# Performance work log

Measured on AMD Instinct MI355X. Metric: run time of the kernel, lower is better.

## Reference

```python
import jax, jax.numpy as jnp
import numpy as np

N, D, NUM_CLASSES = 8192, 1024, 128
ALPHA = 0.1
EPS = 1e-7


def setup_inputs() -> dict:
    key = jax.random.key(0)
    k1, k2 = jax.random.split(key)
    H = jax.random.normal(k1, (N, D), dtype=jnp.float32)
    labels = jax.random.randint(k2, (N,), 0, NUM_CLASSES, dtype=jnp.int64)
    return {"H": H, "labels": labels}


def reference(H, labels):
    n = H.shape[0]
    # squared-euclidean pairwise distances: ||x_i - x_j||^2
    x_norm = jnp.sum(H * H, axis=1)                      # [N]
    dists = x_norm[:, None] + x_norm[None, :] - 2.0 * (H @ H.T)
    dists = jnp.where(jnp.isnan(dists), 0.0, dists)      # dist[dist != dist] = 0
    dists = jnp.maximum(dists, 0.0)                      # clamp(0, inf)
    dists = jnp.maximum(dists, EPS)                      # clamp(min=1e-7)

    diffs = labels[None, :] - labels[:, None]            # [N, N]
    eye = jnp.eye(n, dtype=bool)
    mask_pos = (diffs == 0) & ~eye                       # same label, not self
    mask_neg = diffs != 0                                # different label

    # hardest positive: argmax over positive-masked distances
    anchor_positive_dist = jnp.where(mask_pos, dists, 0.0)
    hardest_positive_idx = jnp.argmax(anchor_positive_dist, axis=1)

    # hard negative: add row-max to non-negatives, take 2nd-smallest (k=1 partition)
    max_neg = jnp.max(dists, axis=1, keepdims=True)
    anchor_negative_dist = dists + max_neg * (1.0 - mask_neg.astype(dists.dtype))
    _, idx2 = jax.lax.top_k(-anchor_negative_dist, 2)    # two smallest per row
    hardest_negatives_idx = idx2[:, 1]

    rows = jnp.arange(n)
    hardest_positive_dist = dists[rows, hardest_positive_idx]
    hardest_negative_dist = dists[rows, hardest_negatives_idx]
    differences = hardest_positive_dist - hardest_negative_dist

    triplet_loss = jnp.maximum(differences + ALPHA, 0.0)  # final='plus', do_max=True
    relevant = triplet_loss > EPS                          # boolean mask (no grad)
    count = jnp.sum(relevant.astype(triplet_loss.dtype))
    return jnp.sum(jnp.where(relevant, triplet_loss, 0.0)) / count
```

## Files before the change

### kernel.cpp

```cpp
#include <hip/hip_runtime.h>
#include <hip/hip_bf16.h>
#include <stdint.h>

constexpr int Nn = 8192;
constexpr int Dd = 1024;
constexpr float kAlpha = 0.1f;
constexpr float kEps = 1e-7f;
constexpr float kInf = 3.0e38f;

constexpr int BM = 128, BN = 128, BK = 32;
constexpr int NB = Nn / BM;
constexpr int NPAIR = NB * (NB + 1) / 2;

using bfx8 = __attribute__((ext_vector_type(8))) __bf16;
using f32x4 = __attribute__((ext_vector_type(4))) float;

__device__ __forceinline__ unsigned short f2bf(float f) {
  union { float f; unsigned int u; } v; v.f = f;
  unsigned int u = v.u;
  u = u + 0x7fffu + ((u >> 16) & 1u);
  return (unsigned short)(u >> 16);
}

__device__ __forceinline__ void min2_insert(float& m1, float& m2, float x) {
  const float lo = fminf(m1, x);
  const float hi = fmaxf(m1, x);
  m1 = lo;
  m2 = fminf(m2, hi);
}

__device__ __forceinline__ void min2_merge(float& m1, float& m2, float o1, float o2) {
  m2 = fminf(fminf(m2, o2), fmaxf(m1, o1));
  m1 = fminf(m1, o1);
}

__global__ __launch_bounds__(256) void prep_kernel(const float* __restrict__ H,
                                                   unsigned short* __restrict__ Hb,
                                                   float* __restrict__ xn) {
  const int wave = threadIdx.x >> 6;
  const int lane = threadIdx.x & 63;
  const int row = blockIdx.x * 4 + wave;
  const float4* src = (const float4*)(H + (size_t)row * Dd);
  ushort4* dst = (ushort4*)(Hb + (size_t)row * Dd);
  float acc = 0.f;
#pragma unroll
  for (int i = 0; i < 4; ++i) {
    float4 v = src[lane + 64 * i];
    acc = fmaf(v.x, v.x, acc);
    acc = fmaf(v.y, v.y, acc);
    acc = fmaf(v.z, v.z, acc);
    acc = fmaf(v.w, v.w, acc);
    ushort4 o;
    o.x = f2bf(v.x); o.y = f2bf(v.y); o.z = f2bf(v.z); o.w = f2bf(v.w);
    dst[lane + 64 * i] = o;
  }
#pragma unroll
  for (int off = 32; off; off >>= 1) acc += __shfl_xor(acc, off, 64);
  if (lane == 0) xn[row] = acc;
}

__global__ __launch_bounds__(256, 3) void triplet_main(
    const unsigned short* __restrict__ Hb, const float* __restrict__ xn,
    const int* __restrict__ lab, float* __restrict__ wsMax,
    float* __restrict__ wsM1, float* __restrict__ wsM2) {
  __shared__ __align__(16) unsigned char smem[16384];
  unsigned short* As = (unsigned short*)smem;
  unsigned short* Bs = (unsigned short*)(smem + 8192);

  const int tid = threadIdx.x;
  const int wave = tid >> 6;
  const int lane = tid & 63;
  const int quad = lane >> 4;
  const int l15 = lane & 15;
  const int wm = wave & 1;
  const int wn = wave >> 1;

  int b = blockIdx.x, I = 0;
  while (b >= NB - I) { b -= NB - I; ++I; }
  const int J = I + b;
  const bool diag = (I == J);

  const int rowBase = I * BM;
  const int colBase = J * BN;

  int lr[16]; float xr[16];
#pragma unroll
  for (int m = 0; m < 4; ++m)
#pragma unroll
    for (int r = 0; r < 4; ++r) {
      const int row = rowBase + wm * 64 + m * 16 + quad * 4 + r;
      lr[m * 4 + r] = lab[row];
      xr[m * 4 + r] = xn[row];
    }

  float maxp[16], mn1[16], mn2[16];
#pragma unroll
  for (int s = 0; s < 16; ++s) { maxp[s] = 0.f; mn1[s] = kInf; mn2[s] = kInf; }

  const int stRow = wave * 32 + (lane >> 2);
  const int stCol = (lane & 3) * 8;

  f32x4 acc[4][4];
#pragma unroll
  for (int m = 0; m < 4; ++m)
#pragma unroll
    for (int n = 0; n < 4; ++n) acc[m][n] = {0.f, 0.f, 0.f, 0.f};

  for (int kt = 0; kt < Dd; kt += BK) {
    __syncthreads();
#pragma unroll
    for (int j = 0; j < 2; ++j) {
      const unsigned short* ga =
          Hb + (size_t)(rowBase + stRow + j * 16) * Dd + kt + stCol;
      __builtin_amdgcn_global_load_lds(
          (const __attribute__((address_space(1))) void*)ga,
          (__attribute__((address_space(3))) void*)&As[(wave * 2 + j) * 512],
          16, 0, 0);
      const unsigned short* gb =
          Hb + (size_t)(colBase + stRow + j * 16) * Dd + kt + stCol;
      __builtin_amdgcn_global_load_lds(
          (const __attribute__((address_space(1))) void*)gb,
          (__attribute__((address_space(3))) void*)&Bs[(wave * 2 + j) * 512],
          16, 0, 0);
    }
    __syncthreads();

    bfx8 a[4], bb[4];
#pragma unroll
    for (int m = 0; m < 4; ++m)
      a[m] = *(const bfx8*)&As[(wm * 64 + m * 16 + l15) * BK + quad * 8];
#pragma unroll
    for (int n = 0; n < 4; ++n)
      bb[n] = *(const bfx8*)&Bs[(wn * 64 + n * 16 + l15) * BK + quad * 8];
#pragma unroll
    for (int m = 0; m < 4; ++m)
#pragma unroll
      for (int n = 0; n < 4; ++n)
        acc[m][n] = __builtin_amdgcn_mfma_f32_16x16x32_bf16(a[m], bb[n], acc[m][n], 0, 0, 0);
  }

  int lc[4]; float xc[4];
#pragma unroll
  for (int n = 0; n < 4; ++n) {
    const int col = colBase + wn * 64 + n * 16 + l15;
    lc[n] = lab[col];
    xc[n] = xn[col];
  }
  float tmaxp[4], tmn1[4], tmn2[4];
#pragma unroll
  for (int n = 0; n < 4; ++n) { tmaxp[n] = 0.f; tmn1[n] = kInf; tmn2[n] = kInf; }

  if (!diag) {
#pragma unroll
    for (int m = 0; m < 4; ++m)
#pragma unroll
      for (int n = 0; n < 4; ++n)
#pragma unroll
        for (int r = 0; r < 4; ++r) {
          const int s = m * 4 + r;
          const float d = fmaf(-2.f, acc[m][n][r], xr[s] + xc[n]);
          const bool eq = (lr[s] == lc[n]);
          const float pos = eq ? d : 0.f;
          const float dn = eq ? kInf : d;
          maxp[s] = fmaxf(maxp[s], pos);
          min2_insert(mn1[s], mn2[s], dn);
          tmaxp[n] = fmaxf(tmaxp[n], pos);
          min2_insert(tmn1[n], tmn2[n], dn);
        }
  } else {
#pragma unroll
    for (int m = 0; m < 4; ++m)
#pragma unroll
      for (int n = 0; n < 4; ++n)
#pragma unroll
        for (int r = 0; r < 4; ++r) {
          const int s = m * 4 + r;
          const bool selfp = (wm == wn) && (m == n) && (quad * 4 + r == l15);
          const float d = fmaf(-2.f, acc[m][n][r], xr[s] + xc[n]);
          const bool eq = (lr[s] == lc[n]);
          const float pos = (eq && !selfp) ? d : 0.f;
          const float dn = eq ? kInf : d;
          maxp[s] = fmaxf(maxp[s], pos);
          min2_insert(mn1[s], mn2[s], dn);
        }
  }

#pragma unroll
  for (int off = 1; off < 16; off <<= 1) {
#pragma unroll
    for (int s = 0; s < 16; ++s) {
      const float om = __shfl_xor(maxp[s], off, 64);
      const float o1 = __shfl_xor(mn1[s], off, 64);
      const float o2 = __shfl_xor(mn2[s], off, 64);
      maxp[s] = fmaxf(maxp[s], om);
      min2_merge(mn1[s], mn2[s], o1, o2);
    }
  }

  __syncthreads();
  float* rbuf = (float*)smem;
  float* tbm = ((float*)smem) + 384;
  float* tb1 = tbm + 1024;
  float* tb2 = tb1 + 1024;

  if (wn == 1 && l15 == 0) {
#pragma unroll
    for (int m = 0; m < 4; ++m)
#pragma unroll
      for (int r = 0; r < 4; ++r) {
        const int s = m * 4 + r;
        const int local = m * 16 + quad * 4 + r;
        rbuf[(wm * 64 + local) * 3 + 0] = maxp[s];
        rbuf[(wm * 64 + local) * 3 + 1] = mn1[s];
        rbuf[(wm * 64 + local) * 3 + 2] = mn2[s];
      }
  }
#pragma unroll
  for (int n = 0; n < 4; ++n) {
    const int idx = (((wm * 2 + wn) * 4 + quad) * 4 + n) * 16 + l15;
    tbm[idx] = tmaxp[n];
    tb1[idx] = tmn1[n];
    tb2[idx] = tmn2[n];
  }
  __syncthreads();

  if (wn == 0 && l15 == 0) {
#pragma unroll
    for (int m = 0; m < 4; ++m)
#pragma unroll
      for (int r = 0; r < 4; ++r) {
        const int s = m * 4 + r;
        const int local = m * 16 + quad * 4 + r;
        float om = rbuf[(wm * 64 + local) * 3 + 0];
        float o1 = rbuf[(wm * 64 + local) * 3 + 1];
        float o2 = rbuf[(wm * 64 + local) * 3 + 2];
        const float M = fmaxf(maxp[s], om);
        float a1 = mn1[s], a2 = mn2[s];
        min2_merge(a1, a2, o1, o2);
        const size_t p = ((size_t)(I * NB + J)) * 128 + wm * 64 + local;
        wsMax[p] = M;
        wsM1[p] = a1;
        wsM2[p] = a2;
      }
  }
  if (wm == 0 && !diag) {
    const int tn = lane >> 4;
    const int tl = lane & 15;
    float M = 0.f, a1 = kInf, a2 = kInf;
#pragma unroll
    for (int wm2 = 0; wm2 < 2; ++wm2)
#pragma unroll
      for (int q = 0; q < 4; ++q) {
        const int idx = (((wm2 * 2 + wn) * 4 + q) * 4 + tn) * 16 + tl;
        M = fmaxf(M, tbm[idx]);
        min2_merge(a1, a2, tb1[idx], tb2[idx]);
      }
    const size_t p = ((size_t)(J * NB + I)) * 128 + wn * 64 + lane;
    wsMax[p] = M;
    wsM1[p] = a1;
    wsM2[p] = a2;
  }
}

__global__ __launch_bounds__(128) void merge_kernel(
    const float* __restrict__ wsMax, const float* __restrict__ wsM1,
    const float* __restrict__ wsM2, float* __restrict__ bsum,
    float* __restrict__ bcnt) {
  const int r = threadIdx.x;
  const int bi = blockIdx.x;
  float mp = 0.f, m1 = kInf, m2 = kInf;
#pragma unroll 8
  for (int bj = 0; bj < NB; ++bj) {
    const size_t p = ((size_t)(bi * NB + bj)) * 128 + r;
    mp = fmaxf(mp, wsMax[p]);
    min2_merge(m1, m2, wsM1[p], wsM2[p]);
  }
  const float loss = fmaxf(mp - m2 + kAlpha, 0.f);
  float ls = (loss > kEps) ? loss : 0.f;
  float lc = (loss > kEps) ? 1.f : 0.f;
#pragma unroll
  for (int off = 32; off; off >>= 1) {
    ls += __shfl_down(ls, off, 64);
    lc += __shfl_down(lc, off, 64);
  }
  __shared__ float ss[2], sc[2];
  if ((threadIdx.x & 63) == 0) { ss[threadIdx.x >> 6] = ls; sc[threadIdx.x >> 6] = lc; }
  __syncthreads();
  if (threadIdx.x == 0) {
    bsum[bi] = ss[0] + ss[1];
    bcnt[bi] = sc[0] + sc[1];
  }
}

__global__ __launch_bounds__(64) void final_kernel(const float* __restrict__ bsum,
                                                   const float* __restrict__ bcnt,
                                                   float* __restrict__ out) {
  float s = bsum[threadIdx.x];
  float c = bcnt[threadIdx.x];
#pragma unroll
  for (int off = 32; off; off >>= 1) {
    s += __shfl_down(s, off, 64);
    c += __shfl_down(c, off, 64);
  }
  if (threadIdx.x == 0) out[0] = s / c;
}

extern "C" void kernel_launch(void* const* d_in, const int* in_sizes, int n_in,
                              void* d_out, int out_size, void* d_ws, size_t ws_size,
                              hipStream_t stream) {
  (void)in_sizes; (void)n_in; (void)out_size; (void)ws_size;
  const float* H = (const float*)d_in[0];
  const int* lab = (const int*)d_in[1];
  float* out = (float*)d_out;

  char* ws = (char*)d_ws;
  unsigned short* Hb = (unsigned short*)ws;
  float* xn = (float*)(ws + (size_t)Nn * Dd * sizeof(unsigned short));
  float* wsMax = xn + Nn;
  float* wsM1 = wsMax + NB * NB * 128;
  float* wsM2 = wsM1 + NB * NB * 128;
  float* bsum = wsM2 + NB * NB * 128;
  float* bcnt = bsum + NB;

  prep_kernel<<<Nn / 4, 256, 0, stream>>>(H, Hb, xn);
  triplet_main<<<NPAIR, 256, 0, stream>>>(Hb, xn, lab, wsMax, wsM1, wsM2);
  merge_kernel<<<NB, 128, 0, stream>>>(wsMax, wsM1, wsM2, bsum, bcnt);
  final_kernel<<<1, 64, 0, stream>>>(bsum, bcnt, out);
}
```

Before: 191.2 us.

## Double-buffer LDS tiles in the distance GEMM and parallelize the merge reduction

The main kernel now uses two 16KB LDS buffers, issuing the global-to-LDS loads for the next K tile before running the MFMAs on the current one. This cuts the loop to one barrier per iteration and lets load latency overlap with compute. The launch-bounds occupancy hint rises from 3 to 4 while LDS use doubles, which may add register pressure. The merge kernel is rewritten to spread the reduction over 256 blocks of 256 threads, splitting the column-block loop across 8 thread groups, and the final kernel grows to 256 threads to match.

```diff
diff --git a/kernel.cpp b/kernel.cpp
--- a/kernel.cpp
+++ b/kernel.cpp
@@ -59,13 +59,11 @@
   if (lane == 0) xn[row] = acc;
 }
 
-__global__ __launch_bounds__(256, 3) void triplet_main(
+__global__ __launch_bounds__(256, 4) void triplet_main(
     const unsigned short* __restrict__ Hb, const float* __restrict__ xn,
     const int* __restrict__ lab, float* __restrict__ wsMax,
     float* __restrict__ wsM1, float* __restrict__ wsM2) {
-  __shared__ __align__(16) unsigned char smem[16384];
-  unsigned short* As = (unsigned short*)smem;
-  unsigned short* Bs = (unsigned short*)(smem + 8192);
+  __shared__ __align__(16) unsigned char smem[32768];
 
   const int tid = threadIdx.x;
   const int wave = tid >> 6;
@@ -92,53 +90,6 @@
       lr[m * 4 + r] = lab[row];
       xr[m * 4 + r] = xn[row];
     }
-
-  float maxp[16], mn1[16], mn2[16];
-#pragma unroll
-  for (int s = 0; s < 16; ++s) { maxp[s] = 0.f; mn1[s] = kInf; mn2[s] = kInf; }
-
-  const int stRow = wave * 32 + (lane >> 2);
-  const int stCol = (lane & 3) * 8;
-
-  f32x4 acc[4][4];
-#pragma unroll
-  for (int m = 0; m < 4; ++m)
-#pragma unroll
-    for (int n = 0; n < 4; ++n) acc[m][n] = {0.f, 0.f, 0.f, 0.f};
-
-  for (int kt = 0; kt < Dd; kt += BK) {
-    __syncthreads();
-#pragma unroll
-    for (int j = 0; j < 2; ++j) {
-      const unsigned short* ga =
-          Hb + (size_t)(rowBase + stRow + j * 16) * Dd + kt + stCol;
-      __builtin_amdgcn_global_load_lds(
-          (const __attribute__((address_space(1))) void*)ga,
-          (__attribute__((address_space(3))) void*)&As[(wave * 2 + j) * 512],
-          16, 0, 0);
-      const unsigned short* gb =
-          Hb + (size_t)(colBase + stRow + j * 16) * Dd + kt + stCol;
-      __builtin_amdgcn_global_load_lds(
-          (const __attribute__((address_space(1))) void*)gb,
-          (__attribute__((address_space(3))) void*)&Bs[(wave * 2 + j) * 512],
-          16, 0, 0);
-    }
-    __syncthreads();
-
-    bfx8 a[4], bb[4];
-#pragma unroll
-    for (int m = 0; m < 4; ++m)
-      a[m] = *(const bfx8*)&As[(wm * 64 + m * 16 + l15) * BK + quad * 8];
-#pragma unroll
-    for (int n = 0; n < 4; ++n)
-      bb[n] = *(const bfx8*)&Bs[(wn * 64 + n * 16 + l15) * BK + quad * 8];
-#pragma unroll
-    for (int m = 0; m < 4; ++m)
-#pragma unroll
-      for (int n = 0; n < 4; ++n)
-        acc[m][n] = __builtin_amdgcn_mfma_f32_16x16x32_bf16(a[m], bb[n], acc[m][n], 0, 0, 0);
-  }
-
   int lc[4]; float xc[4];
 #pragma unroll
   for (int n = 0; n < 4; ++n) {
@@ -146,6 +97,61 @@
     lc[n] = lab[col];
     xc[n] = xn[col];
   }
+
+  const int stRow = wave * 32 + (lane >> 2);
+  const int stCol = (lane & 3) * 8;
+  const unsigned short* gA = Hb + (size_t)(rowBase + stRow) * Dd + stCol;
+  const unsigned short* gB = Hb + (size_t)(colBase + stRow) * Dd + stCol;
+
+  auto stage = [&](int buf, int kt) {
+    unsigned short* s = (unsigned short*)(smem + (buf << 14));
+#pragma unroll
+    for (int j = 0; j < 2; ++j) {
+      __builtin_amdgcn_global_load_lds(
+          (const __attribute__((address_space(1))) void*)(gA + j * 16 * Dd + kt),
+          (__attribute__((address_space(3))) void*)&s[(wave * 2 + j) * 512],
+          16, 0, 0);
+      __builtin_amdgcn_global_load_lds(
+          (const __attribute__((address_space(1))) void*)(gB + j * 16 * Dd + kt),
+          (__attribute__((address_space(3))) void*)&s[4096 + (wave * 2 + j) * 512],
+          16, 0, 0);
+    }
+  };
+
+  f32x4 acc[4][4];
+#pragma unroll
+  for (int m = 0; m < 4; ++m)
+#pragma unroll
+    for (int n = 0; n < 4; ++n) acc[m][n] = {0.f, 0.f, 0.f, 0.f};
+
+  stage(0, 0);
+  __syncthreads();
+
+  constexpr int KIT = Dd / BK;
+  for (int it = 0; it < KIT; ++it) {
+    const int cur = it & 1;
+    if (it + 1 < KIT) stage(cur ^ 1, (it + 1) * BK);
+
+    const unsigned short* s = (const unsigned short*)(smem + (cur << 14));
+    bfx8 a[4], bb[4];
+#pragma unroll
+    for (int m = 0; m < 4; ++m)
+      a[m] = *(const bfx8*)&s[(wm * 64 + m * 16 + l15) * BK + quad * 8];
+#pragma unroll
+    for (int n = 0; n < 4; ++n)
+      bb[n] = *(const bfx8*)&s[4096 + (wn * 64 + n * 16 + l15) * BK + quad * 8];
+#pragma unroll
+    for (int m = 0; m < 4; ++m)
+#pragma unroll
+      for (int n = 0; n < 4; ++n)
+        acc[m][n] = __builtin_amdgcn_mfma_f32_16x16x32_bf16(a[m], bb[n], acc[m][n], 0, 0, 0);
+
+    __syncthreads();
+  }
+
+  float maxp[16], mn1[16], mn2[16];
+#pragma unroll
+  for (int s = 0; s < 16; ++s) { maxp[s] = 0.f; mn1[s] = kInf; mn2[s] = kInf; }
   float tmaxp[4], tmn1[4], tmn2[4];
 #pragma unroll
   for (int n = 0; n < 4; ++n) { tmaxp[n] = 0.f; tmn1[n] = kInf; tmn2[n] = kInf; }
@@ -197,7 +203,6 @@
     }
   }
 
-  __syncthreads();
   float* rbuf = (float*)smem;
   float* tbm = ((float*)smem) + 384;
   float* tb1 = tbm + 1024;
@@ -262,39 +267,51 @@
   }
 }
 
-__global__ __launch_bounds__(128) void merge_kernel(
+__global__ __launch_bounds__(256) void merge_kernel(
     const float* __restrict__ wsMax, const float* __restrict__ wsM1,
     const float* __restrict__ wsM2, float* __restrict__ bsum,
     float* __restrict__ bcnt) {
-  const int r = threadIdx.x;
-  const int bi = blockIdx.x;
+  const int rl = threadIdx.x & 31;
+  const int p = threadIdx.x >> 5;
+  const int row = blockIdx.x * 32 + rl;
+  const int bi = row >> 7;
+  const int rr = row & 127;
   float mp = 0.f, m1 = kInf, m2 = kInf;
-#pragma unroll 8
-  for (int bj = 0; bj < NB; ++bj) {
-    const size_t p = ((size_t)(bi * NB + bj)) * 128 + r;
-    mp = fmaxf(mp, wsMax[p]);
-    min2_merge(m1, m2, wsM1[p], wsM2[p]);
-  }
-  const float loss = fmaxf(mp - m2 + kAlpha, 0.f);
-  float ls = (loss > kEps) ? loss : 0.f;
-  float lc = (loss > kEps) ? 1.f : 0.f;
-#pragma unroll
-  for (int off = 32; off; off >>= 1) {
-    ls += __shfl_down(ls, off, 64);
-    lc += __shfl_down(lc, off, 64);
-  }
-  __shared__ float ss[2], sc[2];
-  if ((threadIdx.x & 63) == 0) { ss[threadIdx.x >> 6] = ls; sc[threadIdx.x >> 6] = lc; }
+#pragma unroll
+  for (int k = 0; k < 8; ++k) {
+    const int bj = p * 8 + k;
+    const size_t idx = ((size_t)(bi * NB + bj)) * 128 + rr;
+    mp = fmaxf(mp, wsMax[idx]);
+    min2_merge(m1, m2, wsM1[idx], wsM2[idx]);
+  }
+  __shared__ float sm[8][32], s1[8][32], s2[8][32];
+  sm[p][rl] = mp; s1[p][rl] = m1; s2[p][rl] = m2;
   __syncthreads();
-  if (threadIdx.x == 0) {
-    bsum[bi] = ss[0] + ss[1];
-    bcnt[bi] = sc[0] + sc[1];
-  }
-}
-
-__global__ __launch_bounds__(64) void final_kernel(const float* __restrict__ bsum,
-                                                   const float* __restrict__ bcnt,
-                                                   float* __restrict__ out) {
+  float ls = 0.f, lc = 0.f;
+  if (threadIdx.x < 32) {
+    mp = sm[0][rl]; m1 = s1[0][rl]; m2 = s2[0][rl];
+#pragma unroll
+    for (int q = 1; q < 8; ++q) {
+      mp = fmaxf(mp, sm[q][rl]);
+      min2_merge(m1, m2, s1[q][rl], s2[q][rl]);
+    }
+    const float loss = fmaxf(mp - m2 + kAlpha, 0.f);
+    ls = (loss > kEps) ? loss : 0.f;
+    lc = (loss > kEps) ? 1.f : 0.f;
+  }
+  if (threadIdx.x < 64) {
+#pragma unroll
+    for (int off = 32; off; off >>= 1) {
+      ls += __shfl_down(ls, off, 64);
+      lc += __shfl_down(lc, off, 64);
+    }
+    if (threadIdx.x == 0) { bsum[blockIdx.x] = ls; bcnt[blockIdx.x] = lc; }
+  }
+}
+
+__global__ __launch_bounds__(256) void final_kernel(const float* __restrict__ bsum,
+                                                    const float* __restrict__ bcnt,
+                                                    float* __restrict__ out) {
   float s = bsum[threadIdx.x];
   float c = bcnt[threadIdx.x];
 #pragma unroll
@@ -302,7 +319,12 @@
     s += __shfl_down(s, off, 64);
     c += __shfl_down(c, off, 64);
   }
-  if (threadIdx.x == 0) out[0] = s / c;
+  __shared__ float ss[4], sc[4];
+  const int w = threadIdx.x >> 6;
+  if ((threadIdx.x & 63) == 0) { ss[w] = s; sc[w] = c; }
+  __syncthreads();
+  if (threadIdx.x == 0)
+    out[0] = (ss[0] + ss[1] + ss[2] + ss[3]) / (sc[0] + sc[1] + sc[2] + sc[3]);
 }
 
 extern "C" void kernel_launch(void* const* d_in, const int* in_sizes, int n_in,
@@ -320,10 +342,10 @@
   float* wsM1 = wsMax + NB * NB * 128;
   float* wsM2 = wsM1 + NB * NB * 128;
   float* bsum = wsM2 + NB * NB * 128;
-  float* bcnt = bsum + NB;
+  float* bcnt = bsum + 256;
 
   prep_kernel<<<Nn / 4, 256, 0, stream>>>(H, Hb, xn);
   triplet_main<<<NPAIR, 256, 0, stream>>>(Hb, xn, lab, wsMax, wsM1, wsM2);
-  merge_kernel<<<NB, 128, 0, stream>>>(wsMax, wsM1, wsM2, bsum, bcnt);
-  final_kernel<<<1, 64, 0, stream>>>(bsum, bcnt, out);
-}
+  merge_kernel<<<256, 256, 0, stream>>>(wsMax, wsM1, wsM2, bsum, bcnt);
+  final_kernel<<<1, 256, 0, stream>>>(bsum, bcnt, out);
+}
```

New measurement: 217.8 us. +13.9%, slower.
